# Kernel optimization log

Measured on AMD Instinct MI355X. Metric: run time of the kernel, lower is better.

Reference implementation:

```python
import jax, jax.numpy as jnp
import numpy as np

NUM_NODES = 262144
NUM_GRAPHS = 256
D_MODEL = 256
LOG_2 = float(np.log(2.0))


def setup_inputs() -> dict:
    key = jax.random.key(0)
    k1, k2, k3 = jax.random.split(key, 3)
    l_enc = jax.random.normal(k1, (NUM_NODES, D_MODEL), dtype=jnp.float32)
    g_enc = jax.random.normal(k2, (NUM_GRAPHS, D_MODEL), dtype=jnp.float32)
    batch = jax.random.randint(k3, (NUM_NODES,), 0, NUM_GRAPHS, dtype=jnp.int64)
    return {"l_enc": l_enc, "g_enc": g_enc, "batch": batch}


def reference(l_enc, g_enc, batch):
    # local_global_loss_ with measure='JSD', mask=[] (msk == ones)
    num_nodes = l_enc.shape[0]
    num_graphs = g_enc.shape[0]
    # pos_mask: one-hot of graph id per node; neg_mask is its complement
    pos_mask = jax.nn.one_hot(batch, num_graphs, dtype=l_enc.dtype)  # [N, G]
    neg_mask = 1.0 - pos_mask
    res = jnp.einsum('nd,gd->ng', l_enc, g_enc)                      # [N, G]
    # JSD positive expectation on res*pos_mask (zeros contribute 0)
    Ep = LOG_2 - jax.nn.softplus(-(res * pos_mask))
    # JSD negative expectation on res*neg_mask (zeros contribute 0)
    rq = res * neg_mask
    Eq = jax.nn.softplus(-rq) + rq - LOG_2
    E_pos = jnp.sum(Ep) / num_nodes
    E_neg = jnp.sum(Eq) / (num_nodes * (num_graphs - 1))
    return E_neg - E_pos
```

## Files before the change

### kernel.cpp

```cpp
#include <hip/hip_runtime.h>
#include <hip/hip_bf16.h>

#define N_NODES 262144
#define N_GRAPHS 256
#define DMODEL 256
#define LN2 0.6931471805599453094

typedef __attribute__((ext_vector_type(4))) float f32x4;
typedef __attribute__((ext_vector_type(8))) short short8;

__device__ __forceinline__ short bf(float x) {
    __hip_bfloat16 h = __float2bfloat16(x);
    return __builtin_bit_cast(short, h);
}

__device__ __forceinline__ short8 cvt8(f32x4 lo, f32x4 hi) {
    short8 a;
    a[0] = bf(lo[0]); a[1] = bf(lo[1]); a[2] = bf(lo[2]); a[3] = bf(lo[3]);
    a[4] = bf(hi[0]); a[5] = bf(hi[1]); a[6] = bf(hi[2]); a[7] = bf(hi[3]);
    return a;
}

__device__ __forceinline__ void mfma16(short8 a0, short8 a1, const char* bb,
                                       f32x4* accA, f32x4* accB) {
#pragma unroll
    for (int nt = 0; nt < 8; ++nt) {
        short8 bfrag = *reinterpret_cast<const short8*>(bb + nt * 1024);
        accA[nt] = __builtin_amdgcn_mfma_f32_16x16x32_bf16(a0, bfrag, accA[nt], 0, 0, 0);
        accB[nt] = __builtin_amdgcn_mfma_f32_16x16x32_bf16(a1, bfrag, accB[nt], 0, 0, 0);
    }
}

__device__ __forceinline__ void elem(float r, int col, int bv,
                                     float& Sl2, float& Sl2p, float& Spr) {
    float t = fminf(r, 64.f) * 1.44269504f;
    float l2 = __log2f(1.f + exp2f(t));
    Sl2 += l2;
    float m = (col == bv) ? 1.f : 0.f;
    Sl2p = fmaf(m, l2, Sl2p);
    Spr = fmaf(m, r, Spr);
}

__global__ void pack_b_kernel(const float* __restrict__ g_enc,
                              short* __restrict__ bout) {
    int b = blockIdx.x;
    int lane = threadIdx.x;
    int ks = b >> 4, nt = b & 15;
    int g = nt * 16 + (lane & 15);
    int k = ks * 32 + (lane >> 4) * 8;
    const float* src = g_enc + g * DMODEL + k;
    short8 v;
#pragma unroll
    for (int j = 0; j < 8; ++j) v[j] = bf(src[j]);
    reinterpret_cast<short8*>(bout)[b * 64 + lane] = v;
}

__global__ __launch_bounds__(512, 1) void mvgrl_main(
    const float* __restrict__ l_enc, const int* __restrict__ batch,
    const short* __restrict__ bpack, double* __restrict__ partials) {
    extern __shared__ char lds_raw[];

    const int tid = threadIdx.x;
    const int lane = tid & 63;
    const int wave = tid >> 6;
    const int wrow = wave & 3;
    const int chalf = wave >> 2;

    {
        const short8* bp = reinterpret_cast<const short8*>(bpack);
        short8* lb = reinterpret_cast<short8*>(lds_raw);
#pragma unroll
        for (int c = 0; c < 16; ++c) {
            int chunk = wave + c * 8;
            lb[chunk * 64 + lane] = bp[chunk * 64 + lane];
        }
    }
    __syncthreads();

    const int row_blk = blockIdx.x * 1024;
    const char* ldsB = lds_raw + chalf * 8192 + lane * 16;
    double dS0 = 0.0, dS1 = 0.0, dS2 = 0.0;

    f32x4 se0l, se0h, se1l, se1h, so0l, so0h, so1l, so1h;

    const int kofs = (lane >> 4) * 8;
    const float* arow = l_enc +
        (size_t)(row_blk + wrow * 32 + (lane & 15)) * DMODEL + kofs;
    const float* am1 = arow + 16 * DMODEL;
    se0l = *reinterpret_cast<const f32x4*>(arow + 0);
    se0h = *reinterpret_cast<const f32x4*>(arow + 4);
    se1l = *reinterpret_cast<const f32x4*>(am1 + 0);
    se1h = *reinterpret_cast<const f32x4*>(am1 + 4);
    so0l = *reinterpret_cast<const f32x4*>(arow + 32);
    so0h = *reinterpret_cast<const f32x4*>(arow + 36);
    so1l = *reinterpret_cast<const f32x4*>(am1 + 32);
    so1h = *reinterpret_cast<const f32x4*>(am1 + 36);

#pragma unroll 1
    for (int pass = 0; pass < 8; ++pass) {
        const int rowbase = row_blk + pass * 128 + wrow * 32;
        const int rsub = (lane >> 4) * 4;
        int bvA0 = batch[rowbase + rsub + 0];
        int bvA1 = batch[rowbase + rsub + 1];
        int bvA2 = batch[rowbase + rsub + 2];
        int bvA3 = batch[rowbase + rsub + 3];
        int bvB0 = batch[rowbase + 16 + rsub + 0];
        int bvB1 = batch[rowbase + 16 + rsub + 1];
        int bvB2 = batch[rowbase + 16 + rsub + 2];
        int bvB3 = batch[rowbase + 16 + rsub + 3];

        const float* arow_next = l_enc +
            (size_t)(row_blk + ((pass + 1) & 7) * 128 + wrow * 32 + (lane & 15)) *
                DMODEL + kofs;

        f32x4 accA[8], accB[8];
#pragma unroll
        for (int n = 0; n < 8; ++n) {
            accA[n] = (f32x4){0.f, 0.f, 0.f, 0.f};
            accB[n] = (f32x4){0.f, 0.f, 0.f, 0.f};
        }

#pragma unroll 1
        for (int g = 0; g < 4; ++g) {
            const float* srcE = (g < 3) ? (arow + (2 * g + 2) * 32) : arow_next;
            const float* srcEm1 = srcE + 16 * DMODEL;
            {
                short8 a0 = cvt8(se0l, se0h);
                short8 a1 = cvt8(se1l, se1h);
                se0l = *reinterpret_cast<const f32x4*>(srcE + 0);
                se0h = *reinterpret_cast<const f32x4*>(srcE + 4);
                se1l = *reinterpret_cast<const f32x4*>(srcEm1 + 0);
                se1h = *reinterpret_cast<const f32x4*>(srcEm1 + 4);
                mfma16(a0, a1, ldsB + (size_t)(2 * g) * 16384, accA, accB);
            }
            {
                short8 a0 = cvt8(so0l, so0h);
                short8 a1 = cvt8(so1l, so1h);
                so0l = *reinterpret_cast<const f32x4*>(srcE + 32);
                so0h = *reinterpret_cast<const f32x4*>(srcE + 36);
                so1l = *reinterpret_cast<const f32x4*>(srcEm1 + 32);
                so1h = *reinterpret_cast<const f32x4*>(srcEm1 + 36);
                mfma16(a0, a1, ldsB + (size_t)(2 * g + 1) * 16384, accA, accB);
            }
        }
        arow = arow_next;

        float Sl2 = 0.f, Sl2p = 0.f, Spr = 0.f;
        const int colbase = chalf * 128 + (lane & 15);
#pragma unroll
        for (int nt = 0; nt < 8; ++nt) {
            const int col = colbase + nt * 16;
            f32x4 avA = accA[nt];
            f32x4 avB = accB[nt];
            elem(avA[0], col, bvA0, Sl2, Sl2p, Spr);
            elem(avA[1], col, bvA1, Sl2, Sl2p, Spr);
            elem(avA[2], col, bvA2, Sl2, Sl2p, Spr);
            elem(avA[3], col, bvA3, Sl2, Sl2p, Spr);
            elem(avB[0], col, bvB0, Sl2, Sl2p, Spr);
            elem(avB[1], col, bvB1, Sl2, Sl2p, Spr);
            elem(avB[2], col, bvB2, Sl2, Sl2p, Spr);
            elem(avB[3], col, bvB3, Sl2, Sl2p, Spr);
        }
        dS0 += (double)Sl2;
        dS1 += (double)Sl2p;
        dS2 += (double)Spr;
    }

#pragma unroll
    for (int off = 32; off; off >>= 1) {
        dS0 += __shfl_xor(dS0, off);
        dS1 += __shfl_xor(dS1, off);
        dS2 += __shfl_xor(dS2, off);
    }
    __syncthreads();
    double* red = reinterpret_cast<double*>(lds_raw);
    if (lane == 0) {
        red[wave * 3 + 0] = dS0;
        red[wave * 3 + 1] = dS1;
        red[wave * 3 + 2] = dS2;
    }
    __syncthreads();
    if (tid == 0) {
        double a = 0, b = 0, c = 0;
#pragma unroll
        for (int w = 0; w < 8; ++w) {
            a += red[w * 3 + 0];
            b += red[w * 3 + 1];
            c += red[w * 3 + 2];
        }
        partials[blockIdx.x * 3 + 0] = a;
        partials[blockIdx.x * 3 + 1] = b;
        partials[blockIdx.x * 3 + 2] = c;
    }
}

__global__ void finalize_kernel(const double* __restrict__ p,
                                float* __restrict__ out) {
    int t = threadIdx.x;
    double a = p[t * 3 + 0], b = p[t * 3 + 1], c = p[t * 3 + 2];
#pragma unroll
    for (int off = 32; off; off >>= 1) {
        a += __shfl_xor(a, off);
        b += __shfl_xor(b, off);
        c += __shfl_xor(c, off);
    }
    __shared__ double red[12];
    int lane = t & 63, w = t >> 6;
    if (lane == 0) { red[w * 3] = a; red[w * 3 + 1] = b; red[w * 3 + 2] = c; }
    __syncthreads();
    if (t == 0) {
        double A = 0, B = 0, C = 0;
#pragma unroll
        for (int i = 0; i < 4; ++i) {
            A += red[i * 3]; B += red[i * 3 + 1]; C += red[i * 3 + 2];
        }
        const double NN = (double)N_NODES, GG = (double)N_GRAPHS;
        double Sall_q = LN2 * A - NN * GG * LN2;
        double Spq = LN2 * B - NN * LN2;
        double Spr = C;
        double neg = (Sall_q - Spq) / (NN * (GG - 1.0));
        double pos = (Spr - Spq) / NN;
        out[0] = (float)(neg - pos);
    }
}

extern "C" void kernel_launch(void* const* d_in, const int* in_sizes, int n_in,
                              void* d_out, int out_size, void* d_ws,
                              size_t ws_size, hipStream_t stream) {
    const float* l_enc = (const float*)d_in[0];
    const float* g_enc = (const float*)d_in[1];
    const int* batch = (const int*)d_in[2];
    float* out = (float*)d_out;

    short* bpack = (short*)d_ws;
    double* partials = (double*)((char*)d_ws + 131072);

    (void)hipFuncSetAttribute(reinterpret_cast<const void*>(mvgrl_main),
                              hipFuncAttributeMaxDynamicSharedMemorySize, 131072);

    pack_b_kernel<<<128, 64, 0, stream>>>(g_enc, bpack);
    mvgrl_main<<<256, 512, 131072, stream>>>(l_enc, batch, bpack, partials);
    finalize_kernel<<<1, 256, 0, stream>>>(partials, out);
}
```

Measured before the change: 89.93 us.

## Fuse g_enc packing into main kernel and prefetch full A rows per pass

Drops the separate pack_b kernel: each block converts g_enc to bf16 and writes it into LDS itself, so one launch and its serial dependency go away. The block's first A row loads are issued before that conversion, so they overlap the staging. The wave tile shrinks from 32 rows to 16 rows per pass, with twice as many passes. All 8 k-chunks of the next row are prefetched into registers (16 f32x4). In exchange, every block redoes the g_enc conversion, and there is less MFMA reuse of each B fragment, since one A fragment now serves 8 MFMAs instead of two serving 16.

```diff
diff --git a/kernel.cpp b/kernel.cpp
--- a/kernel.cpp
+++ b/kernel.cpp
@@ -21,13 +21,11 @@
     return a;
 }
 
-__device__ __forceinline__ void mfma16(short8 a0, short8 a1, const char* bb,
-                                       f32x4* accA, f32x4* accB) {
+__device__ __forceinline__ void mfma8(short8 a, const char* bb, f32x4* acc) {
 #pragma unroll
     for (int nt = 0; nt < 8; ++nt) {
         short8 bfrag = *reinterpret_cast<const short8*>(bb + nt * 1024);
-        accA[nt] = __builtin_amdgcn_mfma_f32_16x16x32_bf16(a0, bfrag, accA[nt], 0, 0, 0);
-        accB[nt] = __builtin_amdgcn_mfma_f32_16x16x32_bf16(a1, bfrag, accB[nt], 0, 0, 0);
+        acc[nt] = __builtin_amdgcn_mfma_f32_16x16x32_bf16(a, bfrag, acc[nt], 0, 0, 0);
     }
 }
 
@@ -41,23 +39,9 @@
     Spr = fmaf(m, r, Spr);
 }
 
-__global__ void pack_b_kernel(const float* __restrict__ g_enc,
-                              short* __restrict__ bout) {
-    int b = blockIdx.x;
-    int lane = threadIdx.x;
-    int ks = b >> 4, nt = b & 15;
-    int g = nt * 16 + (lane & 15);
-    int k = ks * 32 + (lane >> 4) * 8;
-    const float* src = g_enc + g * DMODEL + k;
-    short8 v;
-#pragma unroll
-    for (int j = 0; j < 8; ++j) v[j] = bf(src[j]);
-    reinterpret_cast<short8*>(bout)[b * 64 + lane] = v;
-}
-
 __global__ __launch_bounds__(512, 1) void mvgrl_main(
-    const float* __restrict__ l_enc, const int* __restrict__ batch,
-    const short* __restrict__ bpack, double* __restrict__ partials) {
+    const float* __restrict__ l_enc, const float* __restrict__ g_enc,
+    const int* __restrict__ batch, double* __restrict__ partials) {
     extern __shared__ char lds_raw[];
 
     const int tid = threadIdx.x;
@@ -66,100 +50,131 @@
     const int wrow = wave & 3;
     const int chalf = wave >> 2;
 
+    const int row_blk = blockIdx.x * 1024;
+    const int kofs = (lane >> 4) * 8;
+
+    f32x4 A0l, A0h, A1l, A1h, A2l, A2h, A3l, A3h;
+    f32x4 B0l, B0h, B1l, B1h, B2l, B2h, B3l, B3h;
+    const float* arow0 = l_enc +
+        (size_t)(row_blk + wrow * 16 + (lane & 15)) * DMODEL + kofs;
+    A0l = *reinterpret_cast<const f32x4*>(arow0 + 0);
+    A0h = *reinterpret_cast<const f32x4*>(arow0 + 4);
+    A1l = *reinterpret_cast<const f32x4*>(arow0 + 32);
+    A1h = *reinterpret_cast<const f32x4*>(arow0 + 36);
+    A2l = *reinterpret_cast<const f32x4*>(arow0 + 64);
+    A2h = *reinterpret_cast<const f32x4*>(arow0 + 68);
+    A3l = *reinterpret_cast<const f32x4*>(arow0 + 96);
+    A3h = *reinterpret_cast<const f32x4*>(arow0 + 100);
+    B0l = *reinterpret_cast<const f32x4*>(arow0 + 128);
+    B0h = *reinterpret_cast<const f32x4*>(arow0 + 132);
+    B1l = *reinterpret_cast<const f32x4*>(arow0 + 160);
+    B1h = *reinterpret_cast<const f32x4*>(arow0 + 164);
+    B2l = *reinterpret_cast<const f32x4*>(arow0 + 192);
+    B2h = *reinterpret_cast<const f32x4*>(arow0 + 196);
+    B3l = *reinterpret_cast<const f32x4*>(arow0 + 224);
+    B3h = *reinterpret_cast<const f32x4*>(arow0 + 228);
+
     {
-        const short8* bp = reinterpret_cast<const short8*>(bpack);
         short8* lb = reinterpret_cast<short8*>(lds_raw);
-#pragma unroll
-        for (int c = 0; c < 16; ++c) {
-            int chunk = wave + c * 8;
-            lb[chunk * 64 + lane] = bp[chunk * 64 + lane];
-        }
-    }
-    __syncthreads();
-
-    const int row_blk = blockIdx.x * 1024;
+#pragma unroll 2
+        for (int i = 0; i < 16; ++i) {
+            int c = wave + i * 8;
+            int nt = c & 15, ks = c >> 4;
+            int g = nt * 16 + (lane & 15);
+            int k = ks * 32 + (lane >> 4) * 8;
+            const float* src = g_enc + g * DMODEL + k;
+            f32x4 lo = *reinterpret_cast<const f32x4*>(src);
+            f32x4 hi = *reinterpret_cast<const f32x4*>(src + 4);
+            lb[c * 64 + lane] = cvt8(lo, hi);
+        }
+    }
+    __syncthreads();
+
     const char* ldsB = lds_raw + chalf * 8192 + lane * 16;
     double dS0 = 0.0, dS1 = 0.0, dS2 = 0.0;
 
-    f32x4 se0l, se0h, se1l, se1h, so0l, so0h, so1l, so1h;
-
-    const int kofs = (lane >> 4) * 8;
-    const float* arow = l_enc +
-        (size_t)(row_blk + wrow * 32 + (lane & 15)) * DMODEL + kofs;
-    const float* am1 = arow + 16 * DMODEL;
-    se0l = *reinterpret_cast<const f32x4*>(arow + 0);
-    se0h = *reinterpret_cast<const f32x4*>(arow + 4);
-    se1l = *reinterpret_cast<const f32x4*>(am1 + 0);
-    se1h = *reinterpret_cast<const f32x4*>(am1 + 4);
-    so0l = *reinterpret_cast<const f32x4*>(arow + 32);
-    so0h = *reinterpret_cast<const f32x4*>(arow + 36);
-    so1l = *reinterpret_cast<const f32x4*>(am1 + 32);
-    so1h = *reinterpret_cast<const f32x4*>(am1 + 36);
-
 #pragma unroll 1
-    for (int pass = 0; pass < 8; ++pass) {
-        const int rowbase = row_blk + pass * 128 + wrow * 32;
+    for (int pass = 0; pass < 16; ++pass) {
+        const int rowbase = row_blk + pass * 64 + wrow * 16;
         const int rsub = (lane >> 4) * 4;
-        int bvA0 = batch[rowbase + rsub + 0];
-        int bvA1 = batch[rowbase + rsub + 1];
-        int bvA2 = batch[rowbase + rsub + 2];
-        int bvA3 = batch[rowbase + rsub + 3];
-        int bvB0 = batch[rowbase + 16 + rsub + 0];
-        int bvB1 = batch[rowbase + 16 + rsub + 1];
-        int bvB2 = batch[rowbase + 16 + rsub + 2];
-        int bvB3 = batch[rowbase + 16 + rsub + 3];
-
-        const float* arow_next = l_enc +
-            (size_t)(row_blk + ((pass + 1) & 7) * 128 + wrow * 32 + (lane & 15)) *
+        int bv0 = batch[rowbase + rsub + 0];
+        int bv1 = batch[rowbase + rsub + 1];
+        int bv2 = batch[rowbase + rsub + 2];
+        int bv3 = batch[rowbase + rsub + 3];
+
+        const float* anext = l_enc +
+            (size_t)(row_blk + ((pass + 1) & 15) * 64 + wrow * 16 + (lane & 15)) *
                 DMODEL + kofs;
 
-        f32x4 accA[8], accB[8];
-#pragma unroll
-        for (int n = 0; n < 8; ++n) {
-            accA[n] = (f32x4){0.f, 0.f, 0.f, 0.f};
-            accB[n] = (f32x4){0.f, 0.f, 0.f, 0.f};
-        }
+        f32x4 acc[8];
+#pragma unroll
+        for (int n = 0; n < 8; ++n) acc[n] = (f32x4){0.f, 0.f, 0.f, 0.f};
 
 #pragma unroll 1
-        for (int g = 0; g < 4; ++g) {
-            const float* srcE = (g < 3) ? (arow + (2 * g + 2) * 32) : arow_next;
-            const float* srcEm1 = srcE + 16 * DMODEL;
-            {
-                short8 a0 = cvt8(se0l, se0h);
-                short8 a1 = cvt8(se1l, se1h);
-                se0l = *reinterpret_cast<const f32x4*>(srcE + 0);
-                se0h = *reinterpret_cast<const f32x4*>(srcE + 4);
-                se1l = *reinterpret_cast<const f32x4*>(srcEm1 + 0);
-                se1h = *reinterpret_cast<const f32x4*>(srcEm1 + 4);
-                mfma16(a0, a1, ldsB + (size_t)(2 * g) * 16384, accA, accB);
+        for (int g = 0; g < 2; ++g) {
+            if (g == 0) {
+                {
+                    short8 a = cvt8(A0l, A0h);
+                    A0l = *reinterpret_cast<const f32x4*>(anext + 0);
+                    A0h = *reinterpret_cast<const f32x4*>(anext + 4);
+                    mfma8(a, ldsB + 0 * 16384, acc);
+                }
+                {
+                    short8 a = cvt8(A1l, A1h);
+                    A1l = *reinterpret_cast<const f32x4*>(anext + 32);
+                    A1h = *reinterpret_cast<const f32x4*>(anext + 36);
+                    mfma8(a, ldsB + 1 * 16384, acc);
+                }
+                {
+                    short8 a = cvt8(A2l, A2h);
+                    A2l = *reinterpret_cast<const f32x4*>(anext + 64);
+                    A2h = *reinterpret_cast<const f32x4*>(anext + 68);
+                    mfma8(a, ldsB + 2 * 16384, acc);
+                }
+                {
+                    short8 a = cvt8(A3l, A3h);
+                    A3l = *reinterpret_cast<const f32x4*>(anext + 96);
+                    A3h = *reinterpret_cast<const f32x4*>(anext + 100);
+                    mfma8(a, ldsB + 3 * 16384, acc);
+                }
+            } else {
+                {
+                    short8 a = cvt8(B0l, B0h);
+                    B0l = *reinterpret_cast<const f32x4*>(anext + 128);
+                    B0h = *reinterpret_cast<const f32x4*>(anext + 132);
+                    mfma8(a, ldsB + 4 * 16384, acc);
+                }
+                {
+                    short8 a = cvt8(B1l, B1h);
+                    B1l = *reinterpret_cast<const f32x4*>(anext + 160);
+                    B1h = *reinterpret_cast<const f32x4*>(anext + 164);
+                    mfma8(a, ldsB + 5 * 16384, acc);
+                }
+                {
+                    short8 a = cvt8(B2l, B2h);
+                    B2l = *reinterpret_cast<const f32x4*>(anext + 192);
+                    B2h = *reinterpret_cast<const f32x4*>(anext + 196);
+                    mfma8(a, ldsB + 6 * 16384, acc);
+                }
+                {
+                    short8 a = cvt8(B3l, B3h);
+                    B3l = *reinterpret_cast<const f32x4*>(anext + 224);
+                    B3h = *reinterpret_cast<const f32x4*>(anext + 228);
+                    mfma8(a, ldsB + 7 * 16384, acc);
+                }
             }
-            {
-                short8 a0 = cvt8(so0l, so0h);
-                short8 a1 = cvt8(so1l, so1h);
-                so0l = *reinterpret_cast<const f32x4*>(srcE + 32);
-                so0h = *reinterpret_cast<const f32x4*>(srcE + 36);
-                so1l = *reinterpret_cast<const f32x4*>(srcEm1 + 32);
-                so1h = *reinterpret_cast<const f32x4*>(srcEm1 + 36);
-                mfma16(a0, a1, ldsB + (size_t)(2 * g + 1) * 16384, accA, accB);
-            }
-        }
-        arow = arow_next;
+        }
 
         float Sl2 = 0.f, Sl2p = 0.f, Spr = 0.f;
         const int colbase = chalf * 128 + (lane & 15);
 #pragma unroll
         for (int nt = 0; nt < 8; ++nt) {
             const int col = colbase + nt * 16;
-            f32x4 avA = accA[nt];
-            f32x4 avB = accB[nt];
-            elem(avA[0], col, bvA0, Sl2, Sl2p, Spr);
-            elem(avA[1], col, bvA1, Sl2, Sl2p, Spr);
-            elem(avA[2], col, bvA2, Sl2, Sl2p, Spr);
-            elem(avA[3], col, bvA3, Sl2, Sl2p, Spr);
-            elem(avB[0], col, bvB0, Sl2, Sl2p, Spr);
-            elem(avB[1], col, bvB1, Sl2, Sl2p, Spr);
-            elem(avB[2], col, bvB2, Sl2, Sl2p, Spr);
-            elem(avB[3], col, bvB3, Sl2, Sl2p, Spr);
+            f32x4 av = acc[nt];
+            elem(av[0], col, bv0, Sl2, Sl2p, Spr);
+            elem(av[1], col, bv1, Sl2, Sl2p, Spr);
+            elem(av[2], col, bv2, Sl2, Sl2p, Spr);
+            elem(av[3], col, bv3, Sl2, Sl2p, Spr);
         }
         dS0 += (double)Sl2;
         dS1 += (double)Sl2p;
@@ -232,13 +247,11 @@
     const int* batch = (const int*)d_in[2];
     float* out = (float*)d_out;
 
-    short* bpack = (short*)d_ws;
-    double* partials = (double*)((char*)d_ws + 131072);
+    double* partials = (double*)d_ws;
 
     (void)hipFuncSetAttribute(reinterpret_cast<const void*>(mvgrl_main),
                               hipFuncAttributeMaxDynamicSharedMemorySize, 131072);
 
-    pack_b_kernel<<<128, 64, 0, stream>>>(g_enc, bpack);
-    mvgrl_main<<<256, 512, 131072, stream>>>(l_enc, batch, bpack, partials);
+    mvgrl_main<<<256, 512, 131072, stream>>>(l_enc, g_enc, batch, partials);
     finalize_kernel<<<1, 256, 0, stream>>>(partials, out);
 }
```

Measured after the change: 91.59 us. About the same (+1.8%).

## Split column halves across blocks and fuse g_enc packing into main kernel

Applied to the files above, without the earlier changes.

Removes the separate pack kernel: each block now converts its half of g_enc to bf16 directly into LDS, overlapping that with the first l_enc prefetch. The work split changes from 256 blocks of 8 waves (each covering both column halves) to 512 blocks of 4 waves, each handling one column half for 1024 rows, with LDS per block halved to 64KB. Pairs of blocks sharing the same rows are adjacent in launch order, so l_enc is read twice but that second read may hit in L2. The launch overhead of one kernel is removed, at the cost of redundant g_enc conversion per block and doubled A-side conversion work.

```diff
diff --git a/kernel.cpp b/kernel.cpp
--- a/kernel.cpp
+++ b/kernel.cpp
@@ -41,51 +41,24 @@
     Spr = fmaf(m, r, Spr);
 }
 
-__global__ void pack_b_kernel(const float* __restrict__ g_enc,
-                              short* __restrict__ bout) {
-    int b = blockIdx.x;
-    int lane = threadIdx.x;
-    int ks = b >> 4, nt = b & 15;
-    int g = nt * 16 + (lane & 15);
-    int k = ks * 32 + (lane >> 4) * 8;
-    const float* src = g_enc + g * DMODEL + k;
-    short8 v;
-#pragma unroll
-    for (int j = 0; j < 8; ++j) v[j] = bf(src[j]);
-    reinterpret_cast<short8*>(bout)[b * 64 + lane] = v;
-}
-
-__global__ __launch_bounds__(512, 1) void mvgrl_main(
-    const float* __restrict__ l_enc, const int* __restrict__ batch,
-    const short* __restrict__ bpack, double* __restrict__ partials) {
+__global__ __launch_bounds__(256, 1) void mvgrl_main(
+    const float* __restrict__ l_enc, const float* __restrict__ g_enc,
+    const int* __restrict__ batch, double* __restrict__ partials) {
     extern __shared__ char lds_raw[];
 
     const int tid = threadIdx.x;
     const int lane = tid & 63;
     const int wave = tid >> 6;
-    const int wrow = wave & 3;
-    const int chalf = wave >> 2;
-
-    {
-        const short8* bp = reinterpret_cast<const short8*>(bpack);
-        short8* lb = reinterpret_cast<short8*>(lds_raw);
-#pragma unroll
-        for (int c = 0; c < 16; ++c) {
-            int chunk = wave + c * 8;
-            lb[chunk * 64 + lane] = bp[chunk * 64 + lane];
-        }
-    }
-    __syncthreads();
-
-    const int row_blk = blockIdx.x * 1024;
-    const char* ldsB = lds_raw + chalf * 8192 + lane * 16;
-    double dS0 = 0.0, dS1 = 0.0, dS2 = 0.0;
+    const int bid = blockIdx.x;
+
+    const int rg = (bid >> 4) * 8 + (bid & 7);
+    const int chalf = (bid >> 3) & 1;
+    const int row_blk = rg * 1024;
+    const int kofs = (lane >> 4) * 8;
 
     f32x4 se0l, se0h, se1l, se1h, so0l, so0h, so1l, so1h;
-
-    const int kofs = (lane >> 4) * 8;
     const float* arow = l_enc +
-        (size_t)(row_blk + wrow * 32 + (lane & 15)) * DMODEL + kofs;
+        (size_t)(row_blk + wave * 32 + (lane & 15)) * DMODEL + kofs;
     const float* am1 = arow + 16 * DMODEL;
     se0l = *reinterpret_cast<const f32x4*>(arow + 0);
     se0h = *reinterpret_cast<const f32x4*>(arow + 4);
@@ -96,9 +69,28 @@
     so1l = *reinterpret_cast<const f32x4*>(am1 + 32);
     so1h = *reinterpret_cast<const f32x4*>(am1 + 36);
 
+    {
+        short8* lb = reinterpret_cast<short8*>(lds_raw);
+#pragma unroll 2
+        for (int i = 0; i < 16; ++i) {
+            int c = wave + i * 4;
+            int nt = c & 7, ks = c >> 3;
+            int g = chalf * 128 + nt * 16 + (lane & 15);
+            int k = ks * 32 + (lane >> 4) * 8;
+            const float* src = g_enc + g * DMODEL + k;
+            f32x4 lo = *reinterpret_cast<const f32x4*>(src);
+            f32x4 hi = *reinterpret_cast<const f32x4*>(src + 4);
+            lb[c * 64 + lane] = cvt8(lo, hi);
+        }
+    }
+    __syncthreads();
+
+    const char* ldsB = lds_raw + lane * 16;
+    double dS0 = 0.0, dS1 = 0.0, dS2 = 0.0;
+
 #pragma unroll 1
     for (int pass = 0; pass < 8; ++pass) {
-        const int rowbase = row_blk + pass * 128 + wrow * 32;
+        const int rowbase = row_blk + pass * 128 + wave * 32;
         const int rsub = (lane >> 4) * 4;
         int bvA0 = batch[rowbase + rsub + 0];
         int bvA1 = batch[rowbase + rsub + 1];
@@ -110,7 +102,7 @@
         int bvB3 = batch[rowbase + 16 + rsub + 3];
 
         const float* arow_next = l_enc +
-            (size_t)(row_blk + ((pass + 1) & 7) * 128 + wrow * 32 + (lane & 15)) *
+            (size_t)(row_blk + ((pass + 1) & 7) * 128 + wave * 32 + (lane & 15)) *
                 DMODEL + kofs;
 
         f32x4 accA[8], accB[8];
@@ -131,7 +123,7 @@
                 se0h = *reinterpret_cast<const f32x4*>(srcE + 4);
                 se1l = *reinterpret_cast<const f32x4*>(srcEm1 + 0);
                 se1h = *reinterpret_cast<const f32x4*>(srcEm1 + 4);
-                mfma16(a0, a1, ldsB + (size_t)(2 * g) * 16384, accA, accB);
+                mfma16(a0, a1, ldsB + (size_t)(2 * g) * 8192, accA, accB);
             }
             {
                 short8 a0 = cvt8(so0l, so0h);
@@ -140,7 +132,7 @@
                 so0h = *reinterpret_cast<const f32x4*>(srcE + 36);
                 so1l = *reinterpret_cast<const f32x4*>(srcEm1 + 32);
                 so1h = *reinterpret_cast<const f32x4*>(srcEm1 + 36);
-                mfma16(a0, a1, ldsB + (size_t)(2 * g + 1) * 16384, accA, accB);
+                mfma16(a0, a1, ldsB + (size_t)(2 * g + 1) * 8192, accA, accB);
             }
         }
         arow = arow_next;
@@ -183,14 +175,14 @@
     if (tid == 0) {
         double a = 0, b = 0, c = 0;
 #pragma unroll
-        for (int w = 0; w < 8; ++w) {
+        for (int w = 0; w < 4; ++w) {
             a += red[w * 3 + 0];
             b += red[w * 3 + 1];
             c += red[w * 3 + 2];
         }
-        partials[blockIdx.x * 3 + 0] = a;
-        partials[blockIdx.x * 3 + 1] = b;
-        partials[blockIdx.x * 3 + 2] = c;
+        partials[bid * 3 + 0] = a;
+        partials[bid * 3 + 1] = b;
+        partials[bid * 3 + 2] = c;
     }
 }
 
@@ -204,14 +196,14 @@
         b += __shfl_xor(b, off);
         c += __shfl_xor(c, off);
     }
-    __shared__ double red[12];
+    __shared__ double red[24];
     int lane = t & 63, w = t >> 6;
     if (lane == 0) { red[w * 3] = a; red[w * 3 + 1] = b; red[w * 3 + 2] = c; }
     __syncthreads();
     if (t == 0) {
         double A = 0, B = 0, C = 0;
 #pragma unroll
-        for (int i = 0; i < 4; ++i) {
+        for (int i = 0; i < 8; ++i) {
             A += red[i * 3]; B += red[i * 3 + 1]; C += red[i * 3 + 2];
         }
         const double NN = (double)N_NODES, GG = (double)N_GRAPHS;
@@ -232,13 +224,11 @@
     const int* batch = (const int*)d_in[2];
     float* out = (float*)d_out;
 
-    short* bpack = (short*)d_ws;
-    double* partials = (double*)((char*)d_ws + 131072);
+    double* partials = (double*)d_ws;
 
     (void)hipFuncSetAttribute(reinterpret_cast<const void*>(mvgrl_main),
-                              hipFuncAttributeMaxDynamicSharedMemorySize, 131072);
-
-    pack_b_kernel<<<128, 64, 0, stream>>>(g_enc, bpack);
-    mvgrl_main<<<256, 512, 131072, stream>>>(l_enc, batch, bpack, partials);
-    finalize_kernel<<<1, 256, 0, stream>>>(partials, out);
-}
+                              hipFuncAttributeMaxDynamicSharedMemorySize, 65536);
+
+    mvgrl_main<<<512, 256, 65536, stream>>>(l_enc, g_enc, batch, partials);
+    finalize_kernel<<<1, 512, 0, stream>>>(partials, out);
+}
```

New measurement: 111.2 us. 23.7% more time.
